# Kernel optimization log

Measured on AMD Instinct MI355X. Metric: run time of the kernel, lower is better.

Reference implementation:

```python
import jax, jax.numpy as jnp
import numpy as np

NUM_HEADS = 6
KERNEL = 5
EPS = 1e-6


def _neighbor_idx(L, k):
    # NATTEN neighborhood: window start clamped so every query has exactly k neighbors
    starts = jnp.clip(jnp.arange(L) - k // 2, 0, L - k)
    return starts[:, None] + jnp.arange(k)  # [L, k]


def ada_rmsnorm(x, scale, w1, b1, w2, b2):
    # x: [B,C,D,H,W]; RMS over spatial dims, gamma from channel means via small MLP
    rms = jnp.sqrt(jnp.mean(x * x, axis=(2, 3, 4), keepdims=True) + EPS)
    xn = x / rms
    stats = jnp.mean(x, axis=(2, 3, 4))                 # [B,C]
    h = jax.nn.relu(stats @ w1.T + b1)                  # [B,2C]
    gamma = jax.nn.sigmoid(h @ w2.T + b2)               # [B,C]
    return xn * (scale * gamma[:, :, None, None, None])


def reference(x, scale1, n1_w1, n1_b1, n1_w2, n1_b2,
              qkv_w, qkv_b, proj_w, proj_b,
              scale2, n2_w1, n2_b1, n2_w2, n2_b2,
              mlp_w1, mlp_b1, mlp_w2, mlp_b2):
    B, C, D, H, W = x.shape
    nh_, k_ = NUM_HEADS, KERNEL
    hd = C // nh_
    K3 = k_ ** 3

    # --- norm1 + neighborhood attention ---
    h = ada_rmsnorm(x, scale1, n1_w1, n1_b1, n1_w2, n1_b2)
    t = jnp.transpose(h, (0, 2, 3, 4, 1))               # [B,D,H,W,C]
    qkv = t @ qkv_w.T + qkv_b                           # [B,D,H,W,3C]
    q, k, v = jnp.split(qkv, 3, axis=-1)
    q = q.reshape(B, D, H, W, nh_, hd)
    k = k.reshape(B, D, H, W, nh_, hd)
    v = v.reshape(B, D, H, W, nh_, hd)

    iD = _neighbor_idx(D, k_)
    iH = _neighbor_idx(H, k_)
    iW = _neighbor_idx(W, k_)
    nd = iD[:, None, None, :, None, None]               # [D,1,1,k,1,1]
    nhh = iH[None, :, None, None, :, None]              # [1,H,1,1,k,1]
    nw = iW[None, None, :, None, None, :]               # [1,1,W,1,1,k]

    k_nb = k[:, nd, nhh, nw].reshape(B, D, H, W, K3, nh_, hd)
    v_nb = v[:, nd, nhh, nw].reshape(B, D, H, W, K3, nh_, hd)

    scale_qk = hd ** -0.5
    scores = jnp.einsum('bdhwnc,bdhwknc->bdhwnk', q, k_nb) * scale_qk  # [B,D,H,W,heads,K3]
    p = jax.nn.softmax(scores, axis=-1)
    o = jnp.einsum('bdhwnk,bdhwknc->bdhwnc', p, v_nb).reshape(B, D, H, W, C)
    o = o @ proj_w.T + proj_b                            # output projection
    x = x + jnp.transpose(o, (0, 4, 1, 2, 3))

    # --- norm2 + 1x1-conv MLP (GELU exact) ---
    h2 = ada_rmsnorm(x, scale2, n2_w1, n2_b1, n2_w2, n2_b2)
    m = jnp.einsum('oc,bcdhw->bodhw', mlp_w1, h2) + mlp_b1[None, :, None, None, None]
    m = jax.nn.gelu(m, approximate=False)
    m = jnp.einsum('oc,bcdhw->bodhw', mlp_w2, m) + mlp_b2[None, :, None, None, None]
    return x + m


def setup_inputs() -> dict:
    key = jax.random.key(0)
    ks = jax.random.split(key, 16)
    B, C, D, H, W = 1, 192, 16, 16, 16
    hid = 2 * C
    mlp_h = int(4.0 * C)
    s = 0.02
    inp = {
        'x': jax.random.normal(ks[0], (B, C, D, H, W), jnp.float32),
        'scale1': jnp.ones((1, C, 1, 1, 1), jnp.float32),
        'n1_w1': jax.random.normal(ks[1], (hid, C), jnp.float32) * s,
        'n1_b1': jnp.zeros((hid,), jnp.float32),
        'n1_w2': jax.random.normal(ks[2], (C, hid), jnp.float32) * s,
        'n1_b2': jnp.zeros((C,), jnp.float32),
        'qkv_w': jax.random.normal(ks[3], (3 * C, C), jnp.float32) * s,
        'qkv_b': jnp.zeros((3 * C,), jnp.float32),
        'proj_w': jax.random.normal(ks[4], (C, C), jnp.float32) * s,
        'proj_b': jnp.zeros((C,), jnp.float32),
        'scale2': jnp.ones((1, C, 1, 1, 1), jnp.float32),
        'n2_w1': jax.random.normal(ks[5], (hid, C), jnp.float32) * s,
        'n2_b1': jnp.zeros((hid,), jnp.float32),
        'n2_w2': jax.random.normal(ks[6], (C, hid), jnp.float32) * s,
        'n2_b2': jnp.zeros((C,), jnp.float32),
        'mlp_w1': jax.random.normal(ks[7], (mlp_h, C), jnp.float32) * s,
        'mlp_b1': jnp.zeros((mlp_h,), jnp.float32),
        'mlp_w2': jax.random.normal(ks[8], (C, mlp_h), jnp.float32) * s,
        'mlp_b2': jnp.zeros((C,), jnp.float32),
    }
    return inp
```

## Files before the change

kernel.cpp:

```cpp
#include <hip/hip_runtime.h>
#include <hip/hip_bf16.h>
#include <cmath>


#define NPOS 4096
#define C_CH 192

typedef __bf16 bf16x8 __attribute__((ext_vector_type(8)));
typedef __bf16 bf16x4 __attribute__((ext_vector_type(4)));
typedef float  f32x4  __attribute__((ext_vector_type(4)));

__global__ __launch_bounds__(256) void prep_kernel(
    const float* __restrict__ s0, const float* __restrict__ s1,
    const float* __restrict__ s2, const float* __restrict__ s3,
    __bf16* __restrict__ d0, __bf16* __restrict__ d1,
    __bf16* __restrict__ d2, __bf16* __restrict__ d3,
    const float* __restrict__ x, float* __restrict__ sums, float* __restrict__ sumsq)
{
    int b = blockIdx.x;
    if (b < 432) {
        const float* src; __bf16* dst; int base;
        if (b < 108)      { src = s0; dst = d0; base = b; }
        else if (b < 144) { src = s1; dst = d1; base = b - 108; }
        else if (b < 288) { src = s2; dst = d2; base = b - 144; }
        else              { src = s3; dst = d3; base = b - 288; }
        int i = (base * 256 + threadIdx.x) * 4;
        float4 v = *(const float4*)(src + i);
        bf16x4 o = { (__bf16)v.x, (__bf16)v.y, (__bf16)v.z, (__bf16)v.w };
        *(bf16x4*)(dst + i) = o;
        return;
    }
    int c = b - 432;
    const float4* xc = (const float4*)(x + (size_t)c * NPOS);
    float a = 0.f, a2 = 0.f;
    for (int i = threadIdx.x; i < NPOS / 4; i += 256) {
        float4 v = xc[i];
        a  += v.x + v.y + v.z + v.w;
        a2 += v.x * v.x + v.y * v.y + v.z * v.z + v.w * v.w;
    }
    #pragma unroll
    for (int off = 32; off > 0; off >>= 1) {
        a  += __shfl_down(a, off);
        a2 += __shfl_down(a2, off);
    }
    __shared__ float ls[4], ls2[4];
    int wid = threadIdx.x >> 6;
    if ((threadIdx.x & 63) == 0) { ls[wid] = a; ls2[wid] = a2; }
    __syncthreads();
    if (threadIdx.x == 0) {
        float t = 0.f, t2 = 0.f;
        #pragma unroll
        for (int w = 0; w < 4; w++) { t += ls[w]; t2 += ls2[w]; }
        sums[c] = t; sumsq[c] = t2;
    }
}

__global__ __launch_bounds__(256) void stats_kernel(
    const float* __restrict__ x, float* __restrict__ sums, float* __restrict__ sumsq)
{
    int c = blockIdx.x;
    const float4* xc = (const float4*)(x + (size_t)c * NPOS);
    float a = 0.f, a2 = 0.f;
    for (int i = threadIdx.x; i < NPOS / 4; i += 256) {
        float4 v = xc[i];
        a  += v.x + v.y + v.z + v.w;
        a2 += v.x * v.x + v.y * v.y + v.z * v.z + v.w * v.w;
    }
    #pragma unroll
    for (int off = 32; off > 0; off >>= 1) {
        a  += __shfl_down(a, off);
        a2 += __shfl_down(a2, off);
    }
    __shared__ float ls[4], ls2[4];
    int wid = threadIdx.x >> 6;
    if ((threadIdx.x & 63) == 0) { ls[wid] = a; ls2[wid] = a2; }
    __syncthreads();
    if (threadIdx.x == 0) {
        float t = 0.f, t2 = 0.f;
        #pragma unroll
        for (int w = 0; w < 4; w++) { t += ls[w]; t2 += ls2[w]; }
        sums[c] = t; sumsq[c] = t2;
    }
}

__global__ __launch_bounds__(256) void convx_kernel(
    const float* __restrict__ x,
    const float* __restrict__ sums, const float* __restrict__ sumsq,
    const float* __restrict__ scale,
    const float* __restrict__ w1, const float* __restrict__ b1,
    const float* __restrict__ w2, const float* __restrict__ b2,
    __bf16* __restrict__ xb)
{
    __shared__ float stats[C_CH];
    __shared__ float h[384];
    __shared__ float gsl[C_CH];
    __shared__ float lds[192 * 65];
    int t = threadIdx.x;

    if (t < C_CH) stats[t] = sums[t] * (1.0f / (float)NPOS);
    __syncthreads();
    for (int j = t; j < 384; j += 256) {
        float acc = b1[j];
        const float* wr = w1 + (size_t)j * C_CH;
        #pragma unroll 4
        for (int c = 0; c < C_CH; c += 4) {
            float4 w4 = *(const float4*)(wr + c);
            acc += w4.x * stats[c] + w4.y * stats[c + 1] + w4.z * stats[c + 2] + w4.w * stats[c + 3];
        }
        h[j] = fmaxf(acc, 0.0f);
    }
    __syncthreads();
    if (t < C_CH) {
        float acc = b2[t];
        const float* wr = w2 + (size_t)t * 384;
        #pragma unroll 4
        for (int j = 0; j < 384; j += 4) {
            float4 w4 = *(const float4*)(wr + j);
            acc += w4.x * h[j] + w4.y * h[j + 1] + w4.z * h[j + 2] + w4.w * h[j + 3];
        }
        float g = 1.0f / (1.0f + __expf(-acc));
        float rms = sqrtf(sumsq[t] * (1.0f / (float)NPOS) + 1e-6f);
        gsl[t] = scale[t] * g / rms;
    }
    __syncthreads();

    int p0 = blockIdx.x * 64;
    for (int idx = t; idx < 192 * 16; idx += 256) {
        int row = idx >> 4, p4 = idx & 15;
        float4 v = *(const float4*)(x + (size_t)row * NPOS + p0 + p4 * 4);
        float g = gsl[row];
        lds[row * 65 + p4 * 4 + 0] = v.x * g;
        lds[row * 65 + p4 * 4 + 1] = v.y * g;
        lds[row * 65 + p4 * 4 + 2] = v.z * g;
        lds[row * 65 + p4 * 4 + 3] = v.w * g;
    }
    __syncthreads();
    for (int idx = t; idx < 48 * 64; idx += 256) {
        int c4 = idx >> 6, p = idx & 63;
        bf16x4 o;
        #pragma unroll
        for (int j = 0; j < 4; j++) o[j] = (__bf16)lds[(c4 * 4 + j) * 65 + p];
        *(bf16x4*)(xb + (size_t)(p0 + p) * 192 + c4 * 4) = o;
    }
}

template <int K, int EPI>
__global__ __launch_bounds__(256) void gemm_lds(
    const __bf16* __restrict__ W, const float* __restrict__ bias,
    const __bf16* __restrict__ X, void* __restrict__ out,
    const float* __restrict__ resid, int M,
    float* __restrict__ out_kv)
{
    constexpr int KC  = 192;
    constexpr int LDA = 200;
    __shared__ __bf16 al[64 * LDA];
    __shared__ __bf16 bl[64 * LDA];
    int t    = threadIdx.x;
    int lane = t & 63;
    int wv   = t >> 6;
    int r16  = lane & 15;
    int quad = lane >> 4;
    int wvm  = wv >> 1;
    int wvn  = wv & 1;
    int mBase = blockIdx.y * 64;
    int nBase = blockIdx.x * 64;

    f32x4 acc[2][2];
    #pragma unroll
    for (int i = 0; i < 2; i++)
        #pragma unroll
        for (int j = 0; j < 2; j++)
            acc[i][j] = (f32x4){0.f, 0.f, 0.f, 0.f};

    for (int k0 = 0; k0 < K; k0 += KC) {
        #pragma unroll
        for (int it = 0; it < 6; it++) {
            int c = it * 256 + t;
            int row = c / 24, off = c - row * 24;
            bf16x8 va = *(const bf16x8*)(W + (size_t)(mBase + row) * K + k0 + off * 8);
            *(bf16x8*)(al + row * LDA + off * 8) = va;
            bf16x8 vb = *(const bf16x8*)(X + (size_t)(nBase + row) * K + k0 + off * 8);
            *(bf16x8*)(bl + row * LDA + off * 8) = vb;
        }
        __syncthreads();
        #pragma unroll
        for (int ks = 0; ks < KC / 32; ks++) {
            bf16x8 a0 = *(const bf16x8*)(al + (wvm * 32 + r16) * LDA + ks * 32 + quad * 8);
            bf16x8 a1 = *(const bf16x8*)(al + (wvm * 32 + 16 + r16) * LDA + ks * 32 + quad * 8);
            bf16x8 b0 = *(const bf16x8*)(bl + (wvn * 32 + r16) * LDA + ks * 32 + quad * 8);
            bf16x8 b1 = *(const bf16x8*)(bl + (wvn * 32 + 16 + r16) * LDA + ks * 32 + quad * 8);
            acc[0][0] = __builtin_amdgcn_mfma_f32_16x16x32_bf16(a0, b0, acc[0][0], 0, 0, 0);
            acc[0][1] = __builtin_amdgcn_mfma_f32_16x16x32_bf16(a0, b1, acc[0][1], 0, 0, 0);
            acc[1][0] = __builtin_amdgcn_mfma_f32_16x16x32_bf16(a1, b0, acc[1][0], 0, 0, 0);
            acc[1][1] = __builtin_amdgcn_mfma_f32_16x16x32_bf16(a1, b1, acc[1][1], 0, 0, 0);
        }
        __syncthreads();
    }

    #pragma unroll
    for (int rt = 0; rt < 2; rt++) {
        int m0 = mBase + wvm * 32 + rt * 16 + quad * 4;
        float b0 = bias[m0], b1 = bias[m0 + 1], b2 = bias[m0 + 2], b3 = bias[m0 + 3];
        #pragma unroll
        for (int ct = 0; ct < 2; ct++) {
            int n = nBase + wvn * 32 + ct * 16 + r16;
            f32x4 a4 = acc[rt][ct];
            float g0 = a4[0] + b0, g1 = a4[1] + b1, g2 = a4[2] + b2, g3 = a4[3] + b3;
            if (EPI == 0) {
                int sect = m0 / 192;
                int o0 = m0 - sect * 192;
                if (sect == 0) {
                    const float qs = 0.17677669529663687f;
                    *(float4*)((float*)out + (size_t)n * 192 + o0) =
                        make_float4(g0 * qs, g1 * qs, g2 * qs, g3 * qs);
                } else {
                    *(float4*)(out_kv + (size_t)n * 384 + (sect - 1) * 192 + o0) =
                        make_float4(g0, g1, g2, g3);
                }
            } else if (EPI == 2) {
                float* o = (float*)out;
                size_t i0 = (size_t)m0 * NPOS + n;
                o[i0]            = g0 + resid[i0];
                o[i0 + NPOS]     = g1 + resid[i0 + NPOS];
                o[i0 + 2 * NPOS] = g2 + resid[i0 + 2 * NPOS];
                o[i0 + 3 * NPOS] = g3 + resid[i0 + 3 * NPOS];
            } else {
                bf16x4 v;
                v[0] = (__bf16)(0.5f * g0 * (1.0f + erff(g0 * 0.7071067811865475f)));
                v[1] = (__bf16)(0.5f * g1 * (1.0f + erff(g1 * 0.7071067811865475f)));
                v[2] = (__bf16)(0.5f * g2 * (1.0f + erff(g2 * 0.7071067811865475f)));
                v[3] = (__bf16)(0.5f * g3 * (1.0f + erff(g3 * 0.7071067811865475f)));
                *(bf16x4*)((__bf16*)out + (size_t)n * M + m0) = v;
            }
        }
    }
}

__global__ __launch_bounds__(256) void attn_kernel(
    const float* __restrict__ q, const float* __restrict__ kv, __bf16* __restrict__ o)
{
    int t = threadIdx.x;
    int pairIdx = blockIdx.x * 8 + (t >> 5);
    int sg   = (t >> 3) & 3;
    int lane = t & 7;
    int pos = pairIdx / 6;
    int head = pairIdx - pos * 6;
    int wq = pos & 15;
    int hq = (pos >> 4) & 15;
    int dq = pos >> 8;
    int d0 = min(max(dq - 2, 0), 11);
    int h0 = min(max(hq - 2, 0), 11);
    int w0 = min(max(wq - 2, 0), 11);

    const float* kvb = kv + head * 32 + lane * 4;
    float4 q4 = *(const float4*)(q + (size_t)pos * 192 + head * 32 + lane * 4);

    float l = 0.0f;
    float4 acc = make_float4(0.f, 0.f, 0.f, 0.f);

    for (int dh = sg; dh < 25; dh += 4) {
        int di = dh / 5;
        int hi = dh - di * 5;
        int np0 = (d0 + di) * 256 + (h0 + hi) * 16 + w0;
        const float* p = kvb + (size_t)np0 * 384;
        #pragma unroll
        for (int wi = 0; wi < 5; wi++) {
            float4 k4 = *(const float4*)p;
            float4 v4 = *(const float4*)(p + 192);
            float s = q4.x * k4.x + q4.y * k4.y + q4.z * k4.z + q4.w * k4.w;
            s += __shfl_xor(s, 1);
            s += __shfl_xor(s, 2);
            s += __shfl_xor(s, 4);
            float pr = __expf(s);
            l += pr;
            acc.x += pr * v4.x;
            acc.y += pr * v4.y;
            acc.z += pr * v4.z;
            acc.w += pr * v4.w;
            p += 384;
        }
    }

    #pragma unroll
    for (int off = 8; off <= 16; off <<= 1) {
        l     += __shfl_xor(l, off);
        acc.x += __shfl_xor(acc.x, off);
        acc.y += __shfl_xor(acc.y, off);
        acc.z += __shfl_xor(acc.z, off);
        acc.w += __shfl_xor(acc.w, off);
    }

    if (sg == 0) {
        float rl = 1.0f / l;
        bf16x4 ov = { (__bf16)(acc.x * rl), (__bf16)(acc.y * rl),
                      (__bf16)(acc.z * rl), (__bf16)(acc.w * rl) };
        *(bf16x4*)(o + (size_t)pos * 192 + head * 32 + lane * 4) = ov;
    }
}

extern "C" void kernel_launch(void* const* d_in, const int* in_sizes, int n_in,
                              void* d_out, int out_size, void* d_ws, size_t ws_size,
                              hipStream_t stream)
{
    const float* x      = (const float*)d_in[0];
    const float* scale1 = (const float*)d_in[1];
    const float* n1_w1  = (const float*)d_in[2];
    const float* n1_b1  = (const float*)d_in[3];
    const float* n1_w2  = (const float*)d_in[4];
    const float* n1_b2  = (const float*)d_in[5];
    const float* qkv_w  = (const float*)d_in[6];
    const float* qkv_b  = (const float*)d_in[7];
    const float* proj_w = (const float*)d_in[8];
    const float* proj_b = (const float*)d_in[9];
    const float* scale2 = (const float*)d_in[10];
    const float* n2_w1  = (const float*)d_in[11];
    const float* n2_b1  = (const float*)d_in[12];
    const float* n2_w2  = (const float*)d_in[13];
    const float* n2_b2  = (const float*)d_in[14];
    const float* mlp_w1 = (const float*)d_in[15];
    const float* mlp_b1 = (const float*)d_in[16];
    const float* mlp_w2 = (const float*)d_in[17];
    const float* mlp_b2 = (const float*)d_in[18];

    float* ws = (float*)d_ws;
    float*  q_buf  = ws;
    float*  kv_buf = ws + 786432;
    __bf16* m_buf  = (__bf16*)ws;
    __bf16* xb     = (__bf16*)(ws + 2359296);
    __bf16* o_attn = (__bf16*)(ws + 2752512);
    __bf16* qkv_wb = (__bf16*)(ws + 3145728);
    __bf16* proj_wb = qkv_wb + 110592;
    __bf16* m1_wb   = proj_wb + 36864;
    __bf16* m2_wb   = m1_wb + 147456;
    float*  sums   = ws + 3366912;
    float*  sumsq  = sums + 192;

    float* x2 = (float*)d_out;

    prep_kernel<<<624, 256, 0, stream>>>(qkv_w, proj_w, mlp_w1, mlp_w2,
                                         qkv_wb, proj_wb, m1_wb, m2_wb,
                                         x, sums, sumsq);
    convx_kernel<<<64, 256, 0, stream>>>(x, sums, sumsq, scale1,
                                         n1_w1, n1_b1, n1_w2, n1_b2, xb);
    gemm_lds<192, 0><<<dim3(64, 9), 256, 0, stream>>>(qkv_wb, qkv_b, xb, (void*)q_buf, nullptr, 576, kv_buf);
    attn_kernel<<<3072, 256, 0, stream>>>(q_buf, kv_buf, o_attn);
    gemm_lds<192, 2><<<dim3(64, 3), 256, 0, stream>>>(proj_wb, proj_b, o_attn, (void*)x2, x, 192, nullptr);
    stats_kernel<<<192, 256, 0, stream>>>(x2, sums, sumsq);
    convx_kernel<<<64, 256, 0, stream>>>(x2, sums, sumsq, scale2,
                                         n2_w1, n2_b1, n2_w2, n2_b2, xb);
    gemm_lds<192, 3><<<dim3(64, 12), 256, 0, stream>>>(m1_wb, mlp_b1, xb, (void*)m_buf, nullptr, 768, nullptr);
    gemm_lds<768, 2><<<dim3(64, 3), 256, 0, stream>>>(m2_wb, mlp_b2, m_buf, (void*)x2, x2, 192, nullptr);
}
```

Baseline: 204.1 us.

## Fuse channel stats into proj GEMM epilogue and split-K the MLP down-projection

The separate stats kernel after the output projection goes away. Per-channel sum and sum-of-squares are now reduced inside the projection GEMM epilogue with wave shuffles plus global atomics into a buffer that the prep kernel zeroes. The final MLP GEMM (K=768) becomes split-K over 4 z-slices that atomically add into x2, which already holds the residual, with bias added only by slice 0. This removes one launch and raises parallelism for the under-filled final GEMM (192 blocks), at the cost of atomic traffic and a nondeterministic summation order.

```diff
diff --git a/kernel.cpp b/kernel.cpp
--- a/kernel.cpp
+++ b/kernel.cpp
@@ -15,7 +15,8 @@
     const float* __restrict__ s2, const float* __restrict__ s3,
     __bf16* __restrict__ d0, __bf16* __restrict__ d1,
     __bf16* __restrict__ d2, __bf16* __restrict__ d3,
-    const float* __restrict__ x, float* __restrict__ sums, float* __restrict__ sumsq)
+    const float* __restrict__ x, float* __restrict__ sums, float* __restrict__ sumsq,
+    float* __restrict__ stats2zero)
 {
     int b = blockIdx.x;
     if (b < 432) {
@@ -31,34 +32,9 @@
         return;
     }
     int c = b - 432;
-    const float4* xc = (const float4*)(x + (size_t)c * NPOS);
-    float a = 0.f, a2 = 0.f;
-    for (int i = threadIdx.x; i < NPOS / 4; i += 256) {
-        float4 v = xc[i];
-        a  += v.x + v.y + v.z + v.w;
-        a2 += v.x * v.x + v.y * v.y + v.z * v.z + v.w * v.w;
-    }
-    #pragma unroll
-    for (int off = 32; off > 0; off >>= 1) {
-        a  += __shfl_down(a, off);
-        a2 += __shfl_down(a2, off);
-    }
-    __shared__ float ls[4], ls2[4];
-    int wid = threadIdx.x >> 6;
-    if ((threadIdx.x & 63) == 0) { ls[wid] = a; ls2[wid] = a2; }
-    __syncthreads();
-    if (threadIdx.x == 0) {
-        float t = 0.f, t2 = 0.f;
-        #pragma unroll
-        for (int w = 0; w < 4; w++) { t += ls[w]; t2 += ls2[w]; }
-        sums[c] = t; sumsq[c] = t2;
-    }
-}
-
-__global__ __launch_bounds__(256) void stats_kernel(
-    const float* __restrict__ x, float* __restrict__ sums, float* __restrict__ sumsq)
-{
-    int c = blockIdx.x;
+    if (c == 0) {
+        for (int i = threadIdx.x; i < 384; i += 256) stats2zero[i] = 0.0f;
+    }
     const float4* xc = (const float4*)(x + (size_t)c * NPOS);
     float a = 0.f, a2 = 0.f;
     for (int i = threadIdx.x; i < NPOS / 4; i += 256) {
@@ -149,7 +125,8 @@
     const __bf16* __restrict__ W, const float* __restrict__ bias,
     const __bf16* __restrict__ X, void* __restrict__ out,
     const float* __restrict__ resid, int M,
-    float* __restrict__ out_kv)
+    float* __restrict__ out_kv,
+    float* __restrict__ out_sums, float* __restrict__ out_sumsq)
 {
     constexpr int KC  = 192;
     constexpr int LDA = 200;
@@ -172,7 +149,10 @@
         for (int j = 0; j < 2; j++)
             acc[i][j] = (f32x4){0.f, 0.f, 0.f, 0.f};
 
-    for (int k0 = 0; k0 < K; k0 += KC) {
+    int kBeg = (EPI == 4) ? blockIdx.z * 192 : 0;
+    int kEnd = (EPI == 4) ? kBeg + 192 : K;
+
+    for (int k0 = kBeg; k0 < kEnd; k0 += KC) {
         #pragma unroll
         for (int it = 0; it < 6; it++) {
             int c = it * 256 + t;
@@ -197,10 +177,25 @@
         __syncthreads();
     }
 
+    float sv[2][4], sq[2][4];
+    if (EPI == 2) {
+        #pragma unroll
+        for (int rt = 0; rt < 2; rt++)
+            #pragma unroll
+            for (int j = 0; j < 4; j++) { sv[rt][j] = 0.f; sq[rt][j] = 0.f; }
+    }
+
     #pragma unroll
     for (int rt = 0; rt < 2; rt++) {
         int m0 = mBase + wvm * 32 + rt * 16 + quad * 4;
-        float b0 = bias[m0], b1 = bias[m0 + 1], b2 = bias[m0 + 2], b3 = bias[m0 + 3];
+        float b0, b1, b2, b3;
+        if (EPI == 4) {
+            bool z0 = (blockIdx.z == 0);
+            b0 = z0 ? bias[m0] : 0.f;     b1 = z0 ? bias[m0 + 1] : 0.f;
+            b2 = z0 ? bias[m0 + 2] : 0.f; b3 = z0 ? bias[m0 + 3] : 0.f;
+        } else {
+            b0 = bias[m0]; b1 = bias[m0 + 1]; b2 = bias[m0 + 2]; b3 = bias[m0 + 3];
+        }
         #pragma unroll
         for (int ct = 0; ct < 2; ct++) {
             int n = nBase + wvn * 32 + ct * 16 + r16;
@@ -220,10 +215,22 @@
             } else if (EPI == 2) {
                 float* o = (float*)out;
                 size_t i0 = (size_t)m0 * NPOS + n;
-                o[i0]            = g0 + resid[i0];
-                o[i0 + NPOS]     = g1 + resid[i0 + NPOS];
-                o[i0 + 2 * NPOS] = g2 + resid[i0 + 2 * NPOS];
-                o[i0 + 3 * NPOS] = g3 + resid[i0 + 3 * NPOS];
+                float v0 = g0 + resid[i0];
+                float v1 = g1 + resid[i0 + NPOS];
+                float v2 = g2 + resid[i0 + 2 * NPOS];
+                float v3 = g3 + resid[i0 + 3 * NPOS];
+                o[i0] = v0; o[i0 + NPOS] = v1; o[i0 + 2 * NPOS] = v2; o[i0 + 3 * NPOS] = v3;
+                sv[rt][0] += v0; sq[rt][0] += v0 * v0;
+                sv[rt][1] += v1; sq[rt][1] += v1 * v1;
+                sv[rt][2] += v2; sq[rt][2] += v2 * v2;
+                sv[rt][3] += v3; sq[rt][3] += v3 * v3;
+            } else if (EPI == 4) {
+                float* o = (float*)out;
+                size_t i0 = (size_t)m0 * NPOS + n;
+                atomicAdd(o + i0, g0);
+                atomicAdd(o + i0 + NPOS, g1);
+                atomicAdd(o + i0 + 2 * NPOS, g2);
+                atomicAdd(o + i0 + 3 * NPOS, g3);
             } else {
                 bf16x4 v;
                 v[0] = (__bf16)(0.5f * g0 * (1.0f + erff(g0 * 0.7071067811865475f)));
@@ -231,6 +238,25 @@
                 v[2] = (__bf16)(0.5f * g2 * (1.0f + erff(g2 * 0.7071067811865475f)));
                 v[3] = (__bf16)(0.5f * g3 * (1.0f + erff(g3 * 0.7071067811865475f)));
                 *(bf16x4*)((__bf16*)out + (size_t)n * M + m0) = v;
+            }
+        }
+    }
+
+    if (EPI == 2) {
+        #pragma unroll
+        for (int rt = 0; rt < 2; rt++) {
+            #pragma unroll
+            for (int j = 0; j < 4; j++) {
+                float a = sv[rt][j], b = sq[rt][j];
+                a += __shfl_xor(a, 1); a += __shfl_xor(a, 2);
+                a += __shfl_xor(a, 4); a += __shfl_xor(a, 8);
+                b += __shfl_xor(b, 1); b += __shfl_xor(b, 2);
+                b += __shfl_xor(b, 4); b += __shfl_xor(b, 8);
+                if (r16 == 0) {
+                    int m = mBase + wvm * 32 + rt * 16 + quad * 4 + j;
+                    atomicAdd(out_sums + m, a);
+                    atomicAdd(out_sumsq + m, b);
+                }
             }
         }
     }
@@ -334,20 +360,25 @@
     __bf16* m2_wb   = m1_wb + 147456;
     float*  sums   = ws + 3366912;
     float*  sumsq  = sums + 192;
+    float*  sums2  = ws + 3367296;
+    float*  sumsq2 = sums2 + 192;
 
     float* x2 = (float*)d_out;
 
     prep_kernel<<<624, 256, 0, stream>>>(qkv_w, proj_w, mlp_w1, mlp_w2,
                                          qkv_wb, proj_wb, m1_wb, m2_wb,
-                                         x, sums, sumsq);
+                                         x, sums, sumsq, sums2);
     convx_kernel<<<64, 256, 0, stream>>>(x, sums, sumsq, scale1,
                                          n1_w1, n1_b1, n1_w2, n1_b2, xb);
-    gemm_lds<192, 0><<<dim3(64, 9), 256, 0, stream>>>(qkv_wb, qkv_b, xb, (void*)q_buf, nullptr, 576, kv_buf);
+    gemm_lds<192, 0><<<dim3(64, 9), 256, 0, stream>>>(qkv_wb, qkv_b, xb, (void*)q_buf,
+                                                      nullptr, 576, kv_buf, nullptr, nullptr);
     attn_kernel<<<3072, 256, 0, stream>>>(q_buf, kv_buf, o_attn);
-    gemm_lds<192, 2><<<dim3(64, 3), 256, 0, stream>>>(proj_wb, proj_b, o_attn, (void*)x2, x, 192, nullptr);
-    stats_kernel<<<192, 256, 0, stream>>>(x2, sums, sumsq);
-    convx_kernel<<<64, 256, 0, stream>>>(x2, sums, sumsq, scale2,
+    gemm_lds<192, 2><<<dim3(64, 3), 256, 0, stream>>>(proj_wb, proj_b, o_attn, (void*)x2,
+                                                      x, 192, nullptr, sums2, sumsq2);
+    convx_kernel<<<64, 256, 0, stream>>>(x2, sums2, sumsq2, scale2,
                                          n2_w1, n2_b1, n2_w2, n2_b2, xb);
-    gemm_lds<192, 3><<<dim3(64, 12), 256, 0, stream>>>(m1_wb, mlp_b1, xb, (void*)m_buf, nullptr, 768, nullptr);
-    gemm_lds<768, 2><<<dim3(64, 3), 256, 0, stream>>>(m2_wb, mlp_b2, m_buf, (void*)x2, x2, 192, nullptr);
-}
+    gemm_lds<192, 3><<<dim3(64, 12), 256, 0, stream>>>(m1_wb, mlp_b1, xb, (void*)m_buf,
+                                                       nullptr, 768, nullptr, nullptr, nullptr);
+    gemm_lds<768, 4><<<dim3(64, 3, 4), 256, 0, stream>>>(m2_wb, mlp_b2, m_buf, (void*)x2,
+                                                         nullptr, 192, nullptr, nullptr, nullptr);
+}
```

New measurement: 217.3 us. 6.4% more time.

## Fuse adaptive norm into GEMM prologues and channel stats into projection epilogue

Applied to the files above, without the earlier changes.

Removes the standalone convx and stats kernels. Each GEMM block now recomputes the gamma MLP, then loads x, scales it and converts it to bf16 straight into LDS as the B operand. The proj GEMM epilogue accumulates per-channel sum and sum-of-squares through shuffles and atomics into buffers that the prep kernel zeroes. This cuts launches and the xb round trip through memory, at the cost of redundant MLP work in every block (576 and 768 blocks) and atomic contention.

```diff
diff --git a/kernel.cpp b/kernel.cpp
--- a/kernel.cpp
+++ b/kernel.cpp
@@ -15,7 +15,8 @@
     const float* __restrict__ s2, const float* __restrict__ s3,
     __bf16* __restrict__ d0, __bf16* __restrict__ d1,
     __bf16* __restrict__ d2, __bf16* __restrict__ d3,
-    const float* __restrict__ x, float* __restrict__ sums, float* __restrict__ sumsq)
+    const float* __restrict__ x, float* __restrict__ sums, float* __restrict__ sumsq,
+    float* __restrict__ stats2zero)
 {
     int b = blockIdx.x;
     if (b < 432) {
@@ -31,6 +32,9 @@
         return;
     }
     int c = b - 432;
+    if (c == 0) {
+        for (int i = threadIdx.x; i < 384; i += 256) stats2zero[i] = 0.0f;
+    }
     const float4* xc = (const float4*)(x + (size_t)c * NPOS);
     float a = 0.f, a2 = 0.f;
     for (int i = threadIdx.x; i < NPOS / 4; i += 256) {
@@ -55,101 +59,139 @@
     }
 }
 
-__global__ __launch_bounds__(256) void stats_kernel(
-    const float* __restrict__ x, float* __restrict__ sums, float* __restrict__ sumsq)
-{
-    int c = blockIdx.x;
-    const float4* xc = (const float4*)(x + (size_t)c * NPOS);
-    float a = 0.f, a2 = 0.f;
-    for (int i = threadIdx.x; i < NPOS / 4; i += 256) {
-        float4 v = xc[i];
-        a  += v.x + v.y + v.z + v.w;
-        a2 += v.x * v.x + v.y * v.y + v.z * v.z + v.w * v.w;
-    }
-    #pragma unroll
-    for (int off = 32; off > 0; off >>= 1) {
-        a  += __shfl_down(a, off);
-        a2 += __shfl_down(a2, off);
-    }
-    __shared__ float ls[4], ls2[4];
-    int wid = threadIdx.x >> 6;
-    if ((threadIdx.x & 63) == 0) { ls[wid] = a; ls2[wid] = a2; }
-    __syncthreads();
-    if (threadIdx.x == 0) {
-        float t = 0.f, t2 = 0.f;
-        #pragma unroll
-        for (int w = 0; w < 4; w++) { t += ls[w]; t2 += ls2[w]; }
-        sums[c] = t; sumsq[c] = t2;
-    }
-}
-
-__global__ __launch_bounds__(256) void convx_kernel(
+template <int EPI>
+__global__ __launch_bounds__(256) void gemm_norm(
+    const __bf16* __restrict__ W, const float* __restrict__ bias,
     const float* __restrict__ x,
     const float* __restrict__ sums, const float* __restrict__ sumsq,
     const float* __restrict__ scale,
     const float* __restrict__ w1, const float* __restrict__ b1,
     const float* __restrict__ w2, const float* __restrict__ b2,
-    __bf16* __restrict__ xb)
-{
-    __shared__ float stats[C_CH];
-    __shared__ float h[384];
+    void* __restrict__ out, int M, float* __restrict__ out_kv)
+{
+    constexpr int K   = 192;
+    constexpr int LDA = 200;
+    __shared__ __bf16 al[64 * LDA];
+    __shared__ __bf16 bl[64 * LDA];
     __shared__ float gsl[C_CH];
-    __shared__ float lds[192 * 65];
-    int t = threadIdx.x;
-
-    if (t < C_CH) stats[t] = sums[t] * (1.0f / (float)NPOS);
+    int t    = threadIdx.x;
+    int lane = t & 63;
+    int wv   = t >> 6;
+    int r16  = lane & 15;
+    int quad = lane >> 4;
+    int wvm  = wv >> 1;
+    int wvn  = wv & 1;
+    int mBase = blockIdx.y * 64;
+    int nBase = blockIdx.x * 64;
+
+    {
+        float* stats = (float*)al;
+        float* h     = stats + C_CH;
+        if (t < C_CH) stats[t] = sums[t] * (1.0f / (float)NPOS);
+        __syncthreads();
+        for (int j = t; j < 384; j += 256) {
+            float acc = b1[j];
+            const float* wr = w1 + (size_t)j * C_CH;
+            #pragma unroll 4
+            for (int c = 0; c < C_CH; c += 4) {
+                float4 w4 = *(const float4*)(wr + c);
+                acc += w4.x * stats[c] + w4.y * stats[c + 1] + w4.z * stats[c + 2] + w4.w * stats[c + 3];
+            }
+            h[j] = fmaxf(acc, 0.0f);
+        }
+        __syncthreads();
+        if (t < C_CH) {
+            float acc = b2[t];
+            const float* wr = w2 + (size_t)t * 384;
+            #pragma unroll 4
+            for (int j = 0; j < 384; j += 4) {
+                float4 w4 = *(const float4*)(wr + j);
+                acc += w4.x * h[j] + w4.y * h[j + 1] + w4.z * h[j + 2] + w4.w * h[j + 3];
+            }
+            float g = 1.0f / (1.0f + __expf(-acc));
+            float rms = sqrtf(sumsq[t] * (1.0f / (float)NPOS) + 1e-6f);
+            gsl[t] = scale[t] * g / rms;
+        }
+        __syncthreads();
+    }
+
+    #pragma unroll
+    for (int it = 0; it < 6; it++) {
+        int c = it * 256 + t;
+        int row = c / 24, off = c - row * 24;
+        bf16x8 va = *(const bf16x8*)(W + (size_t)(mBase + row) * K + off * 8);
+        *(bf16x8*)(al + row * LDA + off * 8) = va;
+    }
+    #pragma unroll
+    for (int it = 0; it < 12; it++) {
+        int idx = it * 256 + t;
+        int c = idx >> 4, p4 = idx & 15;
+        float4 v = *(const float4*)(x + (size_t)c * NPOS + nBase + p4 * 4);
+        float g = gsl[c];
+        bl[(p4 * 4 + 0) * LDA + c] = (__bf16)(v.x * g);
+        bl[(p4 * 4 + 1) * LDA + c] = (__bf16)(v.y * g);
+        bl[(p4 * 4 + 2) * LDA + c] = (__bf16)(v.z * g);
+        bl[(p4 * 4 + 3) * LDA + c] = (__bf16)(v.w * g);
+    }
     __syncthreads();
-    for (int j = t; j < 384; j += 256) {
-        float acc = b1[j];
-        const float* wr = w1 + (size_t)j * C_CH;
-        #pragma unroll 4
-        for (int c = 0; c < C_CH; c += 4) {
-            float4 w4 = *(const float4*)(wr + c);
-            acc += w4.x * stats[c] + w4.y * stats[c + 1] + w4.z * stats[c + 2] + w4.w * stats[c + 3];
-        }
-        h[j] = fmaxf(acc, 0.0f);
-    }
-    __syncthreads();
-    if (t < C_CH) {
-        float acc = b2[t];
-        const float* wr = w2 + (size_t)t * 384;
-        #pragma unroll 4
-        for (int j = 0; j < 384; j += 4) {
-            float4 w4 = *(const float4*)(wr + j);
-            acc += w4.x * h[j] + w4.y * h[j + 1] + w4.z * h[j + 2] + w4.w * h[j + 3];
-        }
-        float g = 1.0f / (1.0f + __expf(-acc));
-        float rms = sqrtf(sumsq[t] * (1.0f / (float)NPOS) + 1e-6f);
-        gsl[t] = scale[t] * g / rms;
-    }
-    __syncthreads();
-
-    int p0 = blockIdx.x * 64;
-    for (int idx = t; idx < 192 * 16; idx += 256) {
-        int row = idx >> 4, p4 = idx & 15;
-        float4 v = *(const float4*)(x + (size_t)row * NPOS + p0 + p4 * 4);
-        float g = gsl[row];
-        lds[row * 65 + p4 * 4 + 0] = v.x * g;
-        lds[row * 65 + p4 * 4 + 1] = v.y * g;
-        lds[row * 65 + p4 * 4 + 2] = v.z * g;
-        lds[row * 65 + p4 * 4 + 3] = v.w * g;
-    }
-    __syncthreads();
-    for (int idx = t; idx < 48 * 64; idx += 256) {
-        int c4 = idx >> 6, p = idx & 63;
-        bf16x4 o;
-        #pragma unroll
-        for (int j = 0; j < 4; j++) o[j] = (__bf16)lds[(c4 * 4 + j) * 65 + p];
-        *(bf16x4*)(xb + (size_t)(p0 + p) * 192 + c4 * 4) = o;
-    }
-}
-
-template <int K, int EPI>
+
+    f32x4 acc[2][2];
+    #pragma unroll
+    for (int i = 0; i < 2; i++)
+        #pragma unroll
+        for (int j = 0; j < 2; j++)
+            acc[i][j] = (f32x4){0.f, 0.f, 0.f, 0.f};
+
+    #pragma unroll
+    for (int ks = 0; ks < K / 32; ks++) {
+        bf16x8 a0 = *(const bf16x8*)(al + (wvm * 32 + r16) * LDA + ks * 32 + quad * 8);
+        bf16x8 a1 = *(const bf16x8*)(al + (wvm * 32 + 16 + r16) * LDA + ks * 32 + quad * 8);
+        bf16x8 b0 = *(const bf16x8*)(bl + (wvn * 32 + r16) * LDA + ks * 32 + quad * 8);
+        bf16x8 b1 = *(const bf16x8*)(bl + (wvn * 32 + 16 + r16) * LDA + ks * 32 + quad * 8);
+        acc[0][0] = __builtin_amdgcn_mfma_f32_16x16x32_bf16(a0, b0, acc[0][0], 0, 0, 0);
+        acc[0][1] = __builtin_amdgcn_mfma_f32_16x16x32_bf16(a0, b1, acc[0][1], 0, 0, 0);
+        acc[1][0] = __builtin_amdgcn_mfma_f32_16x16x32_bf16(a1, b0, acc[1][0], 0, 0, 0);
+        acc[1][1] = __builtin_amdgcn_mfma_f32_16x16x32_bf16(a1, b1, acc[1][1], 0, 0, 0);
+    }
+
+    #pragma unroll
+    for (int rt = 0; rt < 2; rt++) {
+        int m0 = mBase + wvm * 32 + rt * 16 + quad * 4;
+        float b0 = bias[m0], b1v = bias[m0 + 1], b2v = bias[m0 + 2], b3 = bias[m0 + 3];
+        #pragma unroll
+        for (int ct = 0; ct < 2; ct++) {
+            int n = nBase + wvn * 32 + ct * 16 + r16;
+            f32x4 a4 = acc[rt][ct];
+            float g0 = a4[0] + b0, g1 = a4[1] + b1v, g2 = a4[2] + b2v, g3 = a4[3] + b3;
+            if (EPI == 0) {
+                int sect = m0 / 192;
+                int o0 = m0 - sect * 192;
+                if (sect == 0) {
+                    const float qs = 0.17677669529663687f;
+                    *(float4*)((float*)out + (size_t)n * 192 + o0) =
+                        make_float4(g0 * qs, g1 * qs, g2 * qs, g3 * qs);
+                } else {
+                    *(float4*)(out_kv + (size_t)n * 384 + (sect - 1) * 192 + o0) =
+                        make_float4(g0, g1, g2, g3);
+                }
+            } else {
+                bf16x4 v;
+                v[0] = (__bf16)(0.5f * g0 * (1.0f + erff(g0 * 0.7071067811865475f)));
+                v[1] = (__bf16)(0.5f * g1 * (1.0f + erff(g1 * 0.7071067811865475f)));
+                v[2] = (__bf16)(0.5f * g2 * (1.0f + erff(g2 * 0.7071067811865475f)));
+                v[3] = (__bf16)(0.5f * g3 * (1.0f + erff(g3 * 0.7071067811865475f)));
+                *(bf16x4*)((__bf16*)out + (size_t)n * M + m0) = v;
+            }
+        }
+    }
+}
+
+template <int K, bool STATS>
 __global__ __launch_bounds__(256) void gemm_lds(
     const __bf16* __restrict__ W, const float* __restrict__ bias,
-    const __bf16* __restrict__ X, void* __restrict__ out,
+    const __bf16* __restrict__ X, float* __restrict__ out,
     const float* __restrict__ resid, int M,
-    float* __restrict__ out_kv)
+    float* __restrict__ out_sums, float* __restrict__ out_sumsq)
 {
     constexpr int KC  = 192;
     constexpr int LDA = 200;
@@ -205,32 +247,29 @@
         for (int ct = 0; ct < 2; ct++) {
             int n = nBase + wvn * 32 + ct * 16 + r16;
             f32x4 a4 = acc[rt][ct];
-            float g0 = a4[0] + b0, g1 = a4[1] + b1, g2 = a4[2] + b2, g3 = a4[3] + b3;
-            if (EPI == 0) {
-                int sect = m0 / 192;
-                int o0 = m0 - sect * 192;
-                if (sect == 0) {
-                    const float qs = 0.17677669529663687f;
-                    *(float4*)((float*)out + (size_t)n * 192 + o0) =
-                        make_float4(g0 * qs, g1 * qs, g2 * qs, g3 * qs);
-                } else {
-                    *(float4*)(out_kv + (size_t)n * 384 + (sect - 1) * 192 + o0) =
-                        make_float4(g0, g1, g2, g3);
+            size_t i0 = (size_t)m0 * NPOS + n;
+            float v0 = a4[0] + b0 + resid[i0];
+            float v1 = a4[1] + b1 + resid[i0 + NPOS];
+            float v2 = a4[2] + b2 + resid[i0 + 2 * NPOS];
+            float v3 = a4[3] + b3 + resid[i0 + 3 * NPOS];
+            out[i0] = v0; out[i0 + NPOS] = v1;
+            out[i0 + 2 * NPOS] = v2; out[i0 + 3 * NPOS] = v3;
+            if (STATS) {
+                float sa0 = v0, sq0 = v0 * v0, sa1 = v1, sq1 = v1 * v1;
+                float sa2 = v2, sq2 = v2 * v2, sa3 = v3, sq3 = v3 * v3;
+                #pragma unroll
+                for (int off = 1; off < 16; off <<= 1) {
+                    sa0 += __shfl_xor(sa0, off); sq0 += __shfl_xor(sq0, off);
+                    sa1 += __shfl_xor(sa1, off); sq1 += __shfl_xor(sq1, off);
+                    sa2 += __shfl_xor(sa2, off); sq2 += __shfl_xor(sq2, off);
+                    sa3 += __shfl_xor(sa3, off); sq3 += __shfl_xor(sq3, off);
                 }
-            } else if (EPI == 2) {
-                float* o = (float*)out;
-                size_t i0 = (size_t)m0 * NPOS + n;
-                o[i0]            = g0 + resid[i0];
-                o[i0 + NPOS]     = g1 + resid[i0 + NPOS];
-                o[i0 + 2 * NPOS] = g2 + resid[i0 + 2 * NPOS];
-                o[i0 + 3 * NPOS] = g3 + resid[i0 + 3 * NPOS];
-            } else {
-                bf16x4 v;
-                v[0] = (__bf16)(0.5f * g0 * (1.0f + erff(g0 * 0.7071067811865475f)));
-                v[1] = (__bf16)(0.5f * g1 * (1.0f + erff(g1 * 0.7071067811865475f)));
-                v[2] = (__bf16)(0.5f * g2 * (1.0f + erff(g2 * 0.7071067811865475f)));
-                v[3] = (__bf16)(0.5f * g3 * (1.0f + erff(g3 * 0.7071067811865475f)));
-                *(bf16x4*)((__bf16*)out + (size_t)n * M + m0) = v;
+                if (r16 == 0) {
+                    atomicAdd(out_sums + m0, sa0);     atomicAdd(out_sumsq + m0, sq0);
+                    atomicAdd(out_sums + m0 + 1, sa1); atomicAdd(out_sumsq + m0 + 1, sq1);
+                    atomicAdd(out_sums + m0 + 2, sa2); atomicAdd(out_sumsq + m0 + 2, sq2);
+                    atomicAdd(out_sums + m0 + 3, sa3); atomicAdd(out_sumsq + m0 + 3, sq3);
+                }
             }
         }
     }
@@ -326,7 +365,6 @@
     float*  q_buf  = ws;
     float*  kv_buf = ws + 786432;
     __bf16* m_buf  = (__bf16*)ws;
-    __bf16* xb     = (__bf16*)(ws + 2359296);
     __bf16* o_attn = (__bf16*)(ws + 2752512);
     __bf16* qkv_wb = (__bf16*)(ws + 3145728);
     __bf16* proj_wb = qkv_wb + 110592;
@@ -334,20 +372,23 @@
     __bf16* m2_wb   = m1_wb + 147456;
     float*  sums   = ws + 3366912;
     float*  sumsq  = sums + 192;
+    float*  sums2  = ws + 3367296;
+    float*  sumsq2 = sums2 + 192;
 
     float* x2 = (float*)d_out;
 
     prep_kernel<<<624, 256, 0, stream>>>(qkv_w, proj_w, mlp_w1, mlp_w2,
                                          qkv_wb, proj_wb, m1_wb, m2_wb,
-                                         x, sums, sumsq);
-    convx_kernel<<<64, 256, 0, stream>>>(x, sums, sumsq, scale1,
-                                         n1_w1, n1_b1, n1_w2, n1_b2, xb);
-    gemm_lds<192, 0><<<dim3(64, 9), 256, 0, stream>>>(qkv_wb, qkv_b, xb, (void*)q_buf, nullptr, 576, kv_buf);
+                                         x, sums, sumsq, sums2);
+    gemm_norm<0><<<dim3(64, 9), 256, 0, stream>>>(qkv_wb, qkv_b, x, sums, sumsq, scale1,
+                                                  n1_w1, n1_b1, n1_w2, n1_b2,
+                                                  (void*)q_buf, 576, kv_buf);
     attn_kernel<<<3072, 256, 0, stream>>>(q_buf, kv_buf, o_attn);
-    gemm_lds<192, 2><<<dim3(64, 3), 256, 0, stream>>>(proj_wb, proj_b, o_attn, (void*)x2, x, 192, nullptr);
-    stats_kernel<<<192, 256, 0, stream>>>(x2, sums, sumsq);
-    convx_kernel<<<64, 256, 0, stream>>>(x2, sums, sumsq, scale2,
-                                         n2_w1, n2_b1, n2_w2, n2_b2, xb);
-    gemm_lds<192, 3><<<dim3(64, 12), 256, 0, stream>>>(m1_wb, mlp_b1, xb, (void*)m_buf, nullptr, 768, nullptr);
-    gemm_lds<768, 2><<<dim3(64, 3), 256, 0, stream>>>(m2_wb, mlp_b2, m_buf, (void*)x2, x2, 192, nullptr);
-}
+    gemm_lds<192, true><<<dim3(64, 3), 256, 0, stream>>>(proj_wb, proj_b, o_attn, x2,
+                                                         x, 192, sums2, sumsq2);
+    gemm_norm<3><<<dim3(64, 12), 256, 0, stream>>>(m1_wb, mlp_b1, x2, sums2, sumsq2, scale2,
+                                                   n2_w1, n2_b1, n2_w2, n2_b2,
+                                                   (void*)m_buf, 768, nullptr);
+    gemm_lds<768, false><<<dim3(64, 3), 256, 0, stream>>>(m2_wb, mlp_b2, m_buf, x2,
+                                                          x2, 192, nullptr, nullptr);
+}
```

Measured after the change: 270.7 us. 32.6% more time.
